# Kernel tuning notes

Hardware: AMD Instinct MI355X
Metric: run time of the kernel (lower is better)

## Reference

```python
import jax, jax.numpy as jnp
import numpy as np

K, PS, WS, WT, NHEADS, STRIDE0_A, STRIDE0 = 7, 7, 8, 1, 1, 8, 4
SCALE = STRIDE0_A // STRIDE0  # index-upsampling factor (coarse stride 8 -> fine stride 4)


def _reflect(i, L):
    # dnls-style reflect bounds: i<0 -> -i, i>=L -> 2*(L-1)-i (single reflection suffices here)
    i = jnp.abs(i)
    return jnp.where(i >= L, 2 * (L - 1) - i, i)


def _patch_offsets(ps):
    pr = jnp.arange(ps) - ps // 2
    return jnp.stack(jnp.meshgrid(pr, pr, indexing='ij'), -1).reshape(-1, 2)  # [ps*ps, 2]


def _exact_search(vid0, vid1):
    # coarse windowed patch-product k-NN search (prod_with_heads), stride0_a query grid
    B, T, C, H, W = vid0.shape
    HD, Ch = NHEADS, C // NHEADS
    v0 = jnp.moveaxis(vid0, 2, -1)  # [B,T,H,W,C]
    v1 = jnp.moveaxis(vid1, 2, -1)
    nH, nW = H // STRIDE0_A, W // STRIDE0_A
    qt, qi, qj = [a.reshape(-1) for a in jnp.meshgrid(jnp.arange(T), jnp.arange(nH), jnp.arange(nW), indexing='ij')]
    qh, qw = qi * STRIDE0_A, qj * STRIDE0_A
    Q = qt.shape[0]
    st = 2 * WT + 1  # temporal window, shifted to stay in [0,T)
    t0 = jnp.clip(qt - WT, 0, T - st)
    offs = jnp.arange(WS) - WS // 2  # spatial window offsets, stride1=1
    ct = jnp.broadcast_to((t0[:, None] + jnp.arange(st))[:, :, None, None], (Q, st, WS, WS)).reshape(Q, -1)
    ch = jnp.broadcast_to((qh[:, None] + offs)[:, None, :, None], (Q, st, WS, WS)).reshape(Q, -1)
    cw = jnp.broadcast_to((qw[:, None] + offs)[:, None, None, :], (Q, st, WS, WS)).reshape(Q, -1)
    S = st * WS * WS
    poffs = _patch_offsets(PS)

    def body(acc, off):  # accumulate patch inner products one patch-pixel at a time (memory-light)
        dr, dc = off[0], off[1]
        p0 = v0[:, qt, _reflect(qh + dr, H), _reflect(qw + dc, W)]   # [B,Q,C]
        p1 = v1[:, ct, _reflect(ch + dr, H), _reflect(cw + dc, W)]   # [B,Q,S,C]
        d = jnp.einsum('bqnc,bqsnc->bnqs', p0.reshape(B, Q, HD, Ch), p1.reshape(B, Q, S, HD, Ch))
        return acc + d, None

    dists, _ = jax.lax.scan(jax.checkpoint(body), jnp.zeros((B, HD, Q, S), v0.dtype), poffs)
    vals, idx = jax.lax.top_k(dists, K)  # product search -> largest first
    qsel = jnp.arange(Q)[None, None, :, None]
    inds = jnp.stack([ct[qsel, idx], ch[qsel, idx], cw[qsel, idx]], -1)  # [B,HD,Q,K,3]
    return vals, inds


def _upsample_inds(inds_a, T, H, W):
    # interpolate_inds: replicate coarse inds to the fine stride0 grid, shifted by the
    # fine-query offset relative to its parent coarse query; anchor self at slot 0.
    nH, nW = H // STRIDE0_A, W // STRIDE0_A
    nHf, nWf = H // STRIDE0, W // STRIDE0
    ft, fi, fj = [a.reshape(-1) for a in jnp.meshgrid(jnp.arange(T), jnp.arange(nHf), jnp.arange(nWf), indexing='ij')]
    fh, fw = fi * STRIDE0, fj * STRIDE0
    ci = jnp.clip(fi // SCALE, 0, nH - 1)
    cj = jnp.clip(fj // SCALE, 0, nW - 1)
    qlin = ft * nH * nW + ci * nW + cj
    base = inds_a[:, :, qlin]  # [B,HD,Qf,K,3]
    dh = (fh - ci * STRIDE0_A)[None, None, :, None]
    dw = (fw - cj * STRIDE0_A)[None, None, :, None]
    it = base[..., 0]
    ih = _reflect(base[..., 1] + dh, H)
    iw = _reflect(base[..., 2] + dw, W)
    it = it.at[..., 0].set(ft[None, None, :])  # anchor_self=True
    ih = ih.at[..., 0].set(fh[None, None, :])
    iw = iw.at[..., 0].set(fw[None, None, :])
    return (ft, fh, fw), (it, ih, iw)


def _refine_dists(vid0, vid1, fq, cand):
    # prod_refine with ws_r=1: evaluate the patch product exactly at the given inds
    B, T, C, H, W = vid0.shape
    HD, Ch = NHEADS, C // NHEADS
    ft, fh, fw = fq
    it, ih, iw = cand
    Qf, k = it.shape[2], it.shape[3]
    v0 = jnp.moveaxis(vid0, 2, -1)                                # [B,T,H,W,C]
    v1h = jnp.moveaxis(vid1, 2, -1).reshape(B, T, H, W, HD, Ch)
    bidx = jnp.arange(B)[:, None, None, None]
    hidx = jnp.arange(HD)[None, :, None, None]
    poffs = _patch_offsets(PS)

    def body(acc, off):
        dr, dc = off[0], off[1]
        p0 = v0[:, ft, _reflect(fh + dr, H), _reflect(fw + dc, W)]              # [B,Qf,C]
        p1 = v1h[bidx, it, _reflect(ih + dr, H), _reflect(iw + dc, W), hidx]    # [B,HD,Qf,k,Ch]
        d = jnp.einsum('bqnc,bnqkc->bnqk', p0.reshape(B, Qf, HD, Ch), p1)
        return acc + d, None

    dists, _ = jax.lax.scan(jax.checkpoint(body), jnp.zeros((B, HD, Qf, k), v0.dtype), poffs)
    return dists


def setup_inputs() -> dict:
    key = jax.random.key(0)
    k0, k1 = jax.random.split(key)
    B, T, C, H, W = 1, 3, 64, 192, 192
    vid0 = jax.random.normal(k0, (B, T, C, H, W), dtype=jnp.float32)
    vid1 = jax.random.normal(k1, (B, T, C, H, W), dtype=jnp.float32)
    flows = jnp.zeros((B, T, 2, H, W), dtype=jnp.float32)  # accepted but unused (fflow/bflow=None)
    return {"vid0": vid0, "vid1": vid1, "flows": flows}


def reference(vid0, vid1, flows):
    B, T, C, H, W = vid0.shape
    dists_a, inds_a = _exact_search(vid0, vid1)            # coarse stride0_a search
    fq, cand = _upsample_inds(inds_a, T, H, W)             # interpolate inds to stride0 grid
    dists_f = _refine_dists(vid0, vid1, fq, cand)          # refine (fill) dists at fine inds
    inds_f = jnp.stack(cand, -1)                           # [B,HD,Qf,K,3]
    return dists_f, inds_f
```

## Files before the change

### kernel.cpp

```cpp
#include <hip/hip_runtime.h>
#include <math.h>

#define TT   3
#define CC   64
#define HH   192
#define WW   192
#define HWW  (HH*WW)
#define NHC  24
#define NWC  24
#define QC   1728
#define SC   192
#define NPIX 49
#define KK   7
#define NHF  48
#define NWF  48
#define QF   6912

__device__ __forceinline__ int reflect(int i, int L) {
  i = i < 0 ? -i : i;
  return (i >= L) ? (2 * (L - 1) - i) : i;
}

__global__ void transpose_tchw_thwc(const float* __restrict__ in0,
                                    const float* __restrict__ in1,
                                    float* __restrict__ out0,
                                    float* __restrict__ out1) {
  const float* in = blockIdx.y ? in1 : in0;
  float* out = blockIdx.y ? out1 : out0;
  int b = blockIdx.x;
  int x0 = (b % 3) * 64;
  int ty = b / 3;
  int t = ty / HH, y = ty % HH;

  __shared__ float tile[64][65];
  int lx = threadIdx.x & 63;
  int lc = threadIdx.x >> 6;

  const float* src = in + (size_t)t * CC * HWW + (size_t)y * WW + x0;
#pragma unroll
  for (int i = 0; i < 16; ++i) {
    int c = lc + i * 4;
    tile[c][lx] = src[(size_t)c * HWW + lx];
  }
  __syncthreads();
  float* dst = out + ((size_t)(t * HH + y) * WW + x0) * CC;
#pragma unroll
  for (int i = 0; i < 16; ++i) {
    int x = lc + i * 4;
    dst[(size_t)x * CC + lx] = tile[lx][x];
  }
}

__global__ __launch_bounds__(256, 6) void coarse_fma_kernel(
    const float* __restrict__ v0, const float* __restrict__ v1,
    int* __restrict__ topk) {
  int bid = blockIdx.x;
  int q = (bid & 7) * (QC / 8) + (bid >> 3);
  int qt = q / (NHC * NWC);
  int r = q % (NHC * NWC);
  int qh = (r / NWC) * 8;
  int qw = (r % NWC) * 8;

  __shared__ float4 region4[4 * 196];
  __shared__ float4 qbuf4[16 * 49];
  __shared__ float  dall[SC];
  float* wbuf = (float*)region4;

  int tid = threadIdx.x;
  int s = tid & 63;
  int w = tid >> 6;
  int oi = s >> 3, oj = s & 7;

  int pxb[13];
#pragma unroll
  for (int i = 0; i < 13; ++i) {
    int p = w + 4 * i;
    if (p > 48) p = 48;
    pxb[i] = ((oi + p / 7) * 14 + (oj + p % 7)) * 16;
  }

  {
    const float* b0 = v0 + (size_t)qt * HWW * CC;
    for (int idx = tid; idx < 896; idx += 256) {
      int p = (idx & 7) | ((idx >> 7) << 3);
      int c4 = (idx >> 3) & 15;
      if (p < 49) {
        int ry = reflect(qh + p / 7 - 3, HH);
        int rx = reflect(qw + p % 7 - 3, WW);
        qbuf4[c4 * 49 + p] = *reinterpret_cast<const float4*>(
            b0 + ((size_t)ry * WW + rx) * CC + c4 * 4);
      }
    }
  }

  for (int ct = 0; ct < 3; ++ct) {
    const float* b1 = v1 + (size_t)ct * HWW * CC;
    float acc[13];
#pragma unroll
    for (int i = 0; i < 13; ++i) acc[i] = 0.f;

#pragma unroll
    for (int ph = 0; ph < 4; ++ph) {
      __syncthreads();
      for (int idx = tid; idx < 1024; idx += 256) {
        int px = (idx & 7) | ((idx >> 5) << 3);
        int c4h = (idx >> 3) & 3;
        if (px < 196) {
          int ry = reflect(qh - 7 + px / 14, HH);
          int rx = reflect(qw - 7 + px % 14, WW);
          region4[c4h * 196 + px] = *reinterpret_cast<const float4*>(
              b1 + ((size_t)ry * WW + rx) * CC + (ph * 4 + c4h) * 4);
        }
      }
      __syncthreads();

#pragma unroll
      for (int i = 0; i < 13; ++i) {
        if (i < 12 || w == 0) {
          int p = w + 4 * i;
          const char* rbase = reinterpret_cast<const char*>(region4) + pxb[i];
#pragma unroll
          for (int c4h = 0; c4h < 4; ++c4h) {
            float4 a = qbuf4[(ph * 4 + c4h) * 49 + p];
            float4 b = *reinterpret_cast<const float4*>(rbase + c4h * 3136);
            acc[i] = fmaf(a.x, b.x, acc[i]);
            acc[i] = fmaf(a.y, b.y, acc[i]);
            acc[i] = fmaf(a.z, b.z, acc[i]);
            acc[i] = fmaf(a.w, b.w, acc[i]);
          }
        }
      }
    }

    __syncthreads();
#pragma unroll
    for (int i = 0; i < 13; ++i) {
      if (i < 12 || w == 0) wbuf[s * 49 + (w + 4 * i)] = acc[i];
    }
    __syncthreads();
    if (tid < 64) {
      float a = 0.f;
      const float* wr = wbuf + tid * 49;
      for (int p = 0; p < NPIX; ++p)
        a = __fadd_rn(a, wr[p]);
      dall[ct * 64 + tid] = a;
    }
  }

  __syncthreads();
  if (tid < 64) {
    int lane = tid;
    float v[3] = {dall[lane], dall[lane + 64], dall[lane + 128]};
    int tk = 0;
#pragma unroll
    for (int k = 0; k < KK; ++k) {
      float bv = -INFINITY;
      int bi = 0x7fffffff;
#pragma unroll
      for (int j = 0; j < 3; ++j) {
        if (!((tk >> j) & 1) && v[j] > bv) { bv = v[j]; bi = lane + j * 64; }
      }
#pragma unroll
      for (int off = 32; off > 0; off >>= 1) {
        float ov = __shfl_xor(bv, off, 64);
        int oi2 = __shfl_xor(bi, off, 64);
        if (ov > bv || (ov == bv && oi2 < bi)) { bv = ov; bi = oi2; }
      }
      if ((bi & 63) == lane) tk |= 1 << (bi >> 6);
      if (lane == 0) topk[q * KK + k] = bi;
    }
  }
}

__global__ __launch_bounds__(448, 7) void refine_kernel(
    const float* __restrict__ v0, const float* __restrict__ v1,
    const int* __restrict__ topk, float* __restrict__ out) {
  int bid = blockIdx.x;
  int f = (bid & 7) * (QF / 8) + (bid >> 3);
  int ft = f / (NHF * NWF);
  int r = f % (NHF * NWF);
  int fi = r / NWF, fj = r % NWF;
  int fh = fi * 4, fw = fj * 4;
  int ci = fi >> 1, cj = fj >> 1;
  int dh = (fi & 1) * 4, dw = (fj & 1) * 4;
  int qlin = ft * (NHC * NWC) + ci * NWC + cj;

  int tid = threadIdx.x;
  int lane = tid & 63;
  int k = tid >> 6;

  __shared__ float qs[NPIX * CC];

  {
    const float* b0 = v0 + (size_t)ft * HWW * CC;
#pragma unroll
    for (int i = 0; i < 7; ++i) {
      int idx = tid + i * 448;
      int p = idx >> 6, c = idx & 63;
      int ry = reflect(fh + p / 7 - 3, HH);
      int rx = reflect(fw + p % 7 - 3, WW);
      qs[idx] = b0[((size_t)ry * WW + rx) * CC + c];
    }
  }
  __syncthreads();

  int it, ih, iw;
  if (k == 0) {
    it = ft; ih = fh; iw = fw;
  } else {
    int s = topk[qlin * KK + k];
    int ti = s >> 6;
    int oi = (s >> 3) & 7, oj = s & 7;
    it = ti;
    ih = reflect(ci * 8 + oi - 4 + dh, HH);
    iw = reflect(cj * 8 + oj - 4 + dw, WW);
  }

  const float* b1 = v1 + (size_t)it * HWW * CC;
  float acc = 0.f;
#pragma unroll
  for (int pr = 0; pr < 7; ++pr) {
    int ry = reflect(ih + pr - 3, HH);
    const float* rowp = b1 + (size_t)ry * WW * CC + lane;
    float vals[7];
#pragma unroll
    for (int pc = 0; pc < 7; ++pc) {
      int rx = reflect(iw + pc - 3, WW);
      vals[pc] = rowp[(size_t)rx * CC];
    }
#pragma unroll
    for (int pc = 0; pc < 7; ++pc)
      acc = fmaf(qs[(pr * 7 + pc) * CC + lane], vals[pc], acc);
  }
#pragma unroll
  for (int off = 32; off > 0; off >>= 1)
    acc += __shfl_xor(acc, off, 64);
  if (lane == 0) {
    float* dout = out;
    float* iout = out + (size_t)QF * KK;
    dout[(size_t)f * KK + k] = acc;
    float* ip = iout + ((size_t)f * KK + k) * 3;
    ip[0] = (float)it;
    ip[1] = (float)ih;
    ip[2] = (float)iw;
  }
}

extern "C" void kernel_launch(void* const* d_in, const int* in_sizes, int n_in,
                              void* d_out, int out_size, void* d_ws,
                              size_t ws_size, hipStream_t stream) {
  const float* vid0 = (const float*)d_in[0];
  const float* vid1 = (const float*)d_in[1];
  float* out = (float*)d_out;

  char* ws = (char*)d_ws;
  int* topk = (int*)ws;
  size_t off = (size_t)QC * KK * sizeof(int);
  off = (off + 255) & ~(size_t)255;
  float* v0t = (float*)(ws + off);
  size_t vbytes = (size_t)TT * HWW * CC * sizeof(float);
  float* v1t = (float*)(ws + off + vbytes);

  transpose_tchw_thwc<<<dim3(TT * HH * (WW / 64), 2), 256, 0, stream>>>(
      vid0, vid1, v0t, v1t);
  coarse_fma_kernel<<<QC, 256, 0, stream>>>(v0t, v1t, topk);
  refine_kernel<<<QF, 448, 0, stream>>>(v0t, v1t, topk, out);
}
```

Baseline: 278.8 us.

## Register-block two candidate rows per thread and read query patch from global

Reworks the coarse search work mapping so each thread computes two candidate offsets (rows oi and oi+4) for a subset of patch pixels, reusing each query float4 for two FMAs chains. The query patch shared buffer is removed; query values are loaded directly from global memory (cached) per thread, freeing LDS and raising the occupancy hint to 8 blocks. This trades fewer LDS reads and more occupancy for redundant global/L1 query loads inside the inner loop.

```diff
diff --git a/kernel.cpp b/kernel.cpp
--- a/kernel.cpp
+++ b/kernel.cpp
@@ -51,7 +51,7 @@
   }
 }
 
-__global__ __launch_bounds__(256, 6) void coarse_fma_kernel(
+__global__ __launch_bounds__(256, 8) void coarse_fma_kernel(
     const float* __restrict__ v0, const float* __restrict__ v1,
     int* __restrict__ topk) {
   int bid = blockIdx.x;
@@ -62,42 +62,35 @@
   int qw = (r % NWC) * 8;
 
   __shared__ float4 region4[4 * 196];
-  __shared__ float4 qbuf4[16 * 49];
   __shared__ float  dall[SC];
   float* wbuf = (float*)region4;
 
   int tid = threadIdx.x;
-  int s = tid & 63;
+  int lane = tid & 63;
   int w = tid >> 6;
-  int oi = s >> 3, oj = s & 7;
-
-  int pxb[13];
-#pragma unroll
-  for (int i = 0; i < 13; ++i) {
-    int p = w + 4 * i;
+  int hf = lane >> 5;
+  int sA = lane & 31;
+  int oiA = sA >> 3, oj = sA & 7;
+  int rres = w + 4 * hf;
+
+  const float* b0 = v0 + (size_t)qt * HWW * CC;
+
+  int pxb[7], qoff[7];
+#pragma unroll
+  for (int i = 0; i < 7; ++i) {
+    int p = rres + 8 * i;
     if (p > 48) p = 48;
-    pxb[i] = ((oi + p / 7) * 14 + (oj + p % 7)) * 16;
-  }
-
-  {
-    const float* b0 = v0 + (size_t)qt * HWW * CC;
-    for (int idx = tid; idx < 896; idx += 256) {
-      int p = (idx & 7) | ((idx >> 7) << 3);
-      int c4 = (idx >> 3) & 15;
-      if (p < 49) {
-        int ry = reflect(qh + p / 7 - 3, HH);
-        int rx = reflect(qw + p % 7 - 3, WW);
-        qbuf4[c4 * 49 + p] = *reinterpret_cast<const float4*>(
-            b0 + ((size_t)ry * WW + rx) * CC + c4 * 4);
-      }
-    }
+    pxb[i] = ((oiA + p / 7) * 14 + (oj + p % 7)) * 16;
+    int ry = reflect(qh + p / 7 - 3, HH);
+    int rx = reflect(qw + p % 7 - 3, WW);
+    qoff[i] = (ry * WW + rx) * CC;
   }
 
   for (int ct = 0; ct < 3; ++ct) {
     const float* b1 = v1 + (size_t)ct * HWW * CC;
-    float acc[13];
-#pragma unroll
-    for (int i = 0; i < 13; ++i) acc[i] = 0.f;
+    float accA[7], accB[7];
+#pragma unroll
+    for (int i = 0; i < 7; ++i) { accA[i] = 0.f; accB[i] = 0.f; }
 
 #pragma unroll
     for (int ph = 0; ph < 4; ++ph) {
@@ -115,18 +108,24 @@
       __syncthreads();
 
 #pragma unroll
-      for (int i = 0; i < 13; ++i) {
-        if (i < 12 || w == 0) {
-          int p = w + 4 * i;
+      for (int i = 0; i < 7; ++i) {
+        if (i < 6 || rres == 0) {
           const char* rbase = reinterpret_cast<const char*>(region4) + pxb[i];
+          const float* qb = b0 + qoff[i] + ph * 16;
 #pragma unroll
           for (int c4h = 0; c4h < 4; ++c4h) {
-            float4 a = qbuf4[(ph * 4 + c4h) * 49 + p];
-            float4 b = *reinterpret_cast<const float4*>(rbase + c4h * 3136);
-            acc[i] = fmaf(a.x, b.x, acc[i]);
-            acc[i] = fmaf(a.y, b.y, acc[i]);
-            acc[i] = fmaf(a.z, b.z, acc[i]);
-            acc[i] = fmaf(a.w, b.w, acc[i]);
+            float4 a = *reinterpret_cast<const float4*>(qb + c4h * 4);
+            float4 bA = *reinterpret_cast<const float4*>(rbase + c4h * 3136);
+            float4 bB =
+                *reinterpret_cast<const float4*>(rbase + c4h * 3136 + 896);
+            accA[i] = fmaf(a.x, bA.x, accA[i]);
+            accA[i] = fmaf(a.y, bA.y, accA[i]);
+            accA[i] = fmaf(a.z, bA.z, accA[i]);
+            accA[i] = fmaf(a.w, bA.w, accA[i]);
+            accB[i] = fmaf(a.x, bB.x, accB[i]);
+            accB[i] = fmaf(a.y, bB.y, accB[i]);
+            accB[i] = fmaf(a.z, bB.z, accB[i]);
+            accB[i] = fmaf(a.w, bB.w, accB[i]);
           }
         }
       }
@@ -134,8 +133,12 @@
 
     __syncthreads();
 #pragma unroll
-    for (int i = 0; i < 13; ++i) {
-      if (i < 12 || w == 0) wbuf[s * 49 + (w + 4 * i)] = acc[i];
+    for (int i = 0; i < 7; ++i) {
+      if (i < 6 || rres == 0) {
+        int p = rres + 8 * i;
+        wbuf[sA * 49 + p] = accA[i];
+        wbuf[(sA + 32) * 49 + p] = accB[i];
+      }
     }
     __syncthreads();
     if (tid < 64) {
@@ -149,7 +152,6 @@
 
   __syncthreads();
   if (tid < 64) {
-    int lane = tid;
     float v[3] = {dall[lane], dall[lane + 64], dall[lane + 128]};
     int tk = 0;
 #pragma unroll
```

New measurement: 789.7 us. 183% more time.
